# Performance work log

Measured on AMD Instinct MI355X. Metric: run time of the kernel, lower is better.

Reference implementation:

```python
import jax, jax.numpy as jnp
import numpy as np

B, N, DIM = 32, 3136, 64
H, DH, AGENTS = 8, 8, 49
INNER = H * DH  # 64
SCALE = DH ** -0.5


def setup_inputs() -> dict:
    key = jax.random.key(0)
    ks = jax.random.split(key, 7)
    s = 0.05
    return {
        "x1": jax.random.normal(ks[0], (B, N, DIM), jnp.float32),
        "x2": jax.random.normal(ks[1], (B, N, INNER), jnp.float32),
        "Wq": jax.random.normal(ks[2], (INNER, DIM), jnp.float32) * s,   # to_q (out,in)
        "Wk": jax.random.normal(ks[3], (DIM, INNER), jnp.float32) * s,   # to_k
        "Wv": jax.random.normal(ks[4], (DIM, INNER), jnp.float32) * s,   # to_v
        "Wo": jax.random.normal(ks[5], (2 * DIM, 2 * DIM), jnp.float32) * s,  # to_out linear
        "bo": jax.random.normal(ks[6], (2 * DIM,), jnp.float32) * s,
    }


def _split_heads(t):
    # (b, n, h*d) -> (b, h, n, d)
    b, n, hd = t.shape
    return t.reshape(b, n, H, hd // H).transpose(0, 2, 1, 3)


def reference(x1, x2, Wq, Wk, Wv, Wo, bo):
    b, n, _ = x1.shape
    q = x1 @ Wq.T                      # (b, n, 64)
    k = x2 @ Wk.T                      # (b, n, dim=64)
    v = x2 @ Wv.T
    # AdaptiveAvgPool2d((49, dim)): n % 49 == 0 and channel 64->64 is identity,
    # so pooling is an exact block mean over the sequence axis.
    agent = q.reshape(b, AGENTS, n // AGENTS, q.shape[-1]).mean(axis=2)  # (b, 49, 64)

    agent_h = _split_heads(agent)      # (b, h, 49, d)
    q1 = _split_heads(q)               # (b, h, n, d)
    k_h = _split_heads(k)
    v_h = _split_heads(v)

    # stage 0: agent tokens attend over keys/values (dropout is identity at eval)
    dots0 = jnp.einsum('bhid,bhjd->bhij', agent_h, k_h) * SCALE   # (b,h,49,n)
    attn0 = jax.nn.softmax(dots0, axis=-1)
    out0 = jnp.einsum('bhij,bhjd->bhid', attn0, v_h)              # (b,h,49,d)

    # stage 1: queries attend over agent tokens
    dots1 = jnp.einsum('bhid,bhjd->bhij', q1, agent_h) * SCALE    # (b,h,n,49)
    attn1 = jax.nn.softmax(dots1, axis=-1)
    out1 = jnp.einsum('bhij,bhjd->bhid', attn1, out0)             # (b,h,n,d)

    out1 = out1.transpose(0, 2, 1, 3).reshape(b, n, -1)           # (b,n,64)
    out1 = jnp.concatenate([out1, x1], axis=-1)                   # (b,n,128)
    return out1 @ Wo.T + bo
```

## Files before the change

### kernel.cpp

```cpp
#include <hip/hip_runtime.h>
#include <hip/hip_bf16.h>

#define NB 32
#define NSEQ 3136
#define NDIM 64
#define NH 8
#define NAG 49

static constexpr float kScale = 0.35355339059327378f;
static constexpr float kLog2e = 1.4426950408889634f;

typedef unsigned short us;
typedef __attribute__((ext_vector_type(8))) __bf16 bf16x8;
typedef __attribute__((ext_vector_type(4))) __bf16 bf16x4;
typedef __attribute__((ext_vector_type(2))) _Float16 f16x2;
typedef __attribute__((ext_vector_type(4))) _Float16 f16x4;
typedef __attribute__((ext_vector_type(8))) _Float16 f16x8;
typedef __attribute__((ext_vector_type(4))) float f32x4;

__device__ __forceinline__ float fexp2(float x) {
#if __has_builtin(__builtin_amdgcn_exp2f)
  return __builtin_amdgcn_exp2f(x);
#else
  return exp2f(x);
#endif
}

__device__ __forceinline__ float frcp(float x) {
#if __has_builtin(__builtin_amdgcn_rcpf)
  return __builtin_amdgcn_rcpf(x);
#else
  return 1.f / x;
#endif
}

__device__ __forceinline__ unsigned pk2(float a, float b) {
#if __has_builtin(__builtin_amdgcn_cvt_pkrtz)
  return __builtin_bit_cast(unsigned, __builtin_amdgcn_cvt_pkrtz(a, b));
#else
  f16x2 v = {(_Float16)a, (_Float16)b};
  return __builtin_bit_cast(unsigned, v);
#endif
}

__device__ __forceinline__ bf16x8 ldw8(const float* W, int row, int c0, int ld) {
  const float4* p = (const float4*)(W + (size_t)row * ld + c0);
  float4 v0 = p[0], v1 = p[1];
  bf16x8 r;
  r[0]=(__bf16)v0.x; r[1]=(__bf16)v0.y; r[2]=(__bf16)v0.z; r[3]=(__bf16)v0.w;
  r[4]=(__bf16)v1.x; r[5]=(__bf16)v1.y; r[6]=(__bf16)v1.z; r[7]=(__bf16)v1.w;
  return r;
}

__global__ __launch_bounds__(256) void agent_x1_kernel(
    const float* __restrict__ x1, const float* __restrict__ Wq,
    us* __restrict__ x1bf, us* __restrict__ agf16) {
  __shared__ float red[4][64];
  __shared__ float marr[64];
  const int a = blockIdx.x, b = blockIdx.y, t = threadIdx.x;
  const int i64 = t & 63, cb = t >> 6;

  {
    const float4* s1 = (const float4*)(x1 + ((size_t)(b * NSEQ) + a * 64 + i64) * NDIM + cb * 16);
    float4 v0 = s1[0], v1 = s1[1], v2 = s1[2], v3 = s1[3];
    bf16x8 p0, p1;
    p0[0]=(__bf16)v0.x; p0[1]=(__bf16)v0.y; p0[2]=(__bf16)v0.z; p0[3]=(__bf16)v0.w;
    p0[4]=(__bf16)v1.x; p0[5]=(__bf16)v1.y; p0[6]=(__bf16)v1.z; p0[7]=(__bf16)v1.w;
    p1[0]=(__bf16)v2.x; p1[1]=(__bf16)v2.y; p1[2]=(__bf16)v2.z; p1[3]=(__bf16)v2.w;
    p1[4]=(__bf16)v3.x; p1[5]=(__bf16)v3.y; p1[6]=(__bf16)v3.z; p1[7]=(__bf16)v3.w;
    __bf16* dst = (__bf16*)x1bf;
    *(bf16x8*)(dst + ((((size_t)b * NAG + a) * 8 + cb * 2) * 64 + i64) * 8) = p0;
    *(bf16x8*)(dst + ((((size_t)b * NAG + a) * 8 + cb * 2 + 1) * 64 + i64) * 8) = p1;
  }
  {
    const float* xc = x1 + ((size_t)(b * NSEQ) + a * 64 + cb * 16) * NDIM + i64;
    float cs = 0.f;
#pragma unroll
    for (int i = 0; i < 16; ++i) cs += xc[i * NDIM];
    red[cb][i64] = cs;
  }
  __syncthreads();
  if (t < 64) marr[t] = red[0][t] + red[1][t] + red[2][t] + red[3][t];
  __syncthreads();
  if (t < 64) {
    const float4* wqr = (const float4*)(Wq + (size_t)t * NDIM);
    const float4* mm = (const float4*)marr;
    float s0 = 0.f;
#pragma unroll
    for (int i = 0; i < 16; ++i) {
      float4 wv4 = wqr[i], m4 = mm[i];
      s0 += wv4.x * m4.x + wv4.y * m4.y + wv4.z * m4.z + wv4.w * m4.w;
    }
    const float val = s0 * (kScale * kLog2e / 64.f);
    ((_Float16*)agf16)[(((size_t)b * NH + (t >> 3)) * NAG + a) * 8 + (t & 7)] =
        (_Float16)val;
  }
}

__global__ __launch_bounds__(256) void kv_stage0_kernel(
    const float* __restrict__ x2, const float* __restrict__ Wk,
    const float* __restrict__ Wv, const us* __restrict__ agf16,
    float* __restrict__ pvp) {
  __shared__ __align__(16) __bf16 xb[64][72];
  __shared__ __align__(16) _Float16 klds[4][64][24];
  __shared__ __align__(16) _Float16 vlds[4][18][72];
  __shared__ __align__(16) _Float16 plds[4][64][40];
  const int a = blockIdx.x, b = blockIdx.y, t = threadIdx.x;
  const int i64 = t & 63, cb = t >> 6;
  const int w = cb, lr = (t >> 4) & 3, lc = t & 15;

  bf16x8 ak0 = ldw8(Wk, w * 16 + lc, lr * 8, NDIM);
  bf16x8 ak1 = ldw8(Wk, w * 16 + lc, 32 + lr * 8, NDIM);
  bf16x8 av0 = ldw8(Wv, w * 16 + lc, lr * 8, NDIM);
  bf16x8 av1 = ldw8(Wv, w * 16 + lc, 32 + lr * 8, NDIM);

  {
    const float4* s2 = (const float4*)(x2 + ((size_t)(b * NSEQ) + a * 64 + i64) * NDIM + cb * 16);
    float4 v0 = s2[0], v1 = s2[1], v2 = s2[2], v3 = s2[3];
    bf16x8 p0, p1;
    p0[0]=(__bf16)v0.x; p0[1]=(__bf16)v0.y; p0[2]=(__bf16)v0.z; p0[3]=(__bf16)v0.w;
    p0[4]=(__bf16)v1.x; p0[5]=(__bf16)v1.y; p0[6]=(__bf16)v1.z; p0[7]=(__bf16)v1.w;
    p1[0]=(__bf16)v2.x; p1[1]=(__bf16)v2.y; p1[2]=(__bf16)v2.z; p1[3]=(__bf16)v2.w;
    p1[4]=(__bf16)v3.x; p1[5]=(__bf16)v3.y; p1[6]=(__bf16)v3.z; p1[7]=(__bf16)v3.w;
    *(bf16x8*)&xb[i64][cb * 16] = p0; *(bf16x8*)&xb[i64][cb * 16 + 8] = p1;
  }
  __syncthreads();

  f32x4 acck[4], accv[4];
#pragma unroll
  for (int i = 0; i < 4; ++i) {
    acck[i] = (f32x4){0.f, 0.f, 0.f, 0.f};
    accv[i] = (f32x4){0.f, 0.f, 0.f, 0.f};
  }
#pragma unroll
  for (int nt = 0; nt < 4; ++nt) {
    bf16x8 x0 = *(const bf16x8*)&xb[nt * 16 + lc][lr * 8];
    bf16x8 x1f = *(const bf16x8*)&xb[nt * 16 + lc][32 + lr * 8];
    acck[nt] = __builtin_amdgcn_mfma_f32_16x16x32_bf16(ak0, x0, acck[nt], 0, 0, 0);
    acck[nt] = __builtin_amdgcn_mfma_f32_16x16x32_bf16(ak1, x1f, acck[nt], 0, 0, 0);
    accv[nt] = __builtin_amdgcn_mfma_f32_16x16x32_bf16(av0, x0, accv[nt], 0, 0, 0);
    accv[nt] = __builtin_amdgcn_mfma_f32_16x16x32_bf16(av1, x1f, accv[nt], 0, 0, 0);
  }
#pragma unroll
  for (int nt = 0; nt < 4; ++nt) {
    f16x4 pk4;
    pk4[0]=(_Float16)acck[nt][0]; pk4[1]=(_Float16)acck[nt][1];
    pk4[2]=(_Float16)acck[nt][2]; pk4[3]=(_Float16)acck[nt][3];
    *(f16x4*)&klds[w][nt * 16 + lc][lr * 4] = pk4;
#pragma unroll
    for (int j = 0; j < 4; ++j)
      vlds[w][lr * 4 + j][nt * 16 + lc] = (_Float16)accv[nt][j];
  }
  vlds[w][16][i64] = (_Float16)1.0f;

  const size_t bh0 = (size_t)b * NH + 2 * w;
  f16x8 ba[2][4];
#pragma unroll
  for (int hh = 0; hh < 2; ++hh)
#pragma unroll
    for (int at = 0; at < 4; ++at) {
      f16x8 v = (f16x8)(_Float16)0.0f;
      if (lr == 0) {
        int row = at * 16 + lc; if (row > 48) row = 48;
        v = *(const f16x8*)(agf16 + (bh0 + hh) * (NAG * 8) + row * 8);
      }
      ba[hh][at] = v;
    }

#pragma unroll
  for (int hh = 0; hh < 2; ++hh) {
    f32x4 accPV[4];
#pragma unroll
    for (int i = 0; i < 4; ++i) accPV[i] = (f32x4){0.f, 0.f, 0.f, 0.f};
#pragma unroll
    for (int half = 0; half < 2; ++half) {
#pragma unroll
      for (int tb = 0; tb < 2; ++tb) {
        const int tokbase = half * 32 + tb * 16;
        f16x8 kf = *(const f16x8*)&klds[w][tokbase + lc][hh * 8];
#pragma unroll
        for (int at = 0; at < 4; ++at) {
          f32x4 sc = __builtin_amdgcn_mfma_f32_16x16x32_f16(
              kf, ba[hh][at], (f32x4){0.f, 0.f, 0.f, 0.f}, 0, 0, 0);
          unsigned u0 = pk2(fexp2(sc[0]), fexp2(sc[1]));
          unsigned u1 = pk2(fexp2(sc[2]), fexp2(sc[3]));
          unsigned long long q = ((unsigned long long)u1 << 32) | u0;
          *(unsigned long long*)&plds[w][at * 16 + lc][tb * 16 + lr * 4] = q;
        }
      }
      const int frow = (lc < 8) ? hh * 8 + lc : 16;
      f16x8 vf = *(const f16x8*)&vlds[w][frow][half * 32 + lr * 8];
#pragma unroll
      for (int at = 0; at < 4; ++at) {
        f16x8 pf = *(const f16x8*)&plds[w][at * 16 + lc][lr * 8];
        accPV[at] = __builtin_amdgcn_mfma_f32_16x16x32_f16(pf, vf, accPV[at], 0, 0, 0);
      }
    }
    if (lc < 9) {
      float* dst = pvp + ((size_t)a * (NB * NH) + bh0 + hh) * 441;
#pragma unroll
      for (int at = 0; at < 4; ++at)
#pragma unroll
        for (int j = 0; j < 4; ++j) {
          const int ag = at * 16 + lr * 4 + j;
          if (ag < NAG) dst[ag * 9 + lc] = accPV[at][j];
        }
    }
  }
}

__global__ __launch_bounds__(256) void aofin_kernel(
    const float* __restrict__ pvp, us* __restrict__ pvtF) {
  __shared__ float acc[441];
  const int h = blockIdx.x, b = blockIdx.y, t = threadIdx.x;
  const size_t bh = (size_t)b * NH + h;
  for (int s = t; s < 441; s += 256) {
    float v = 0.f;
#pragma unroll 7
    for (int aa = 0; aa < NAG; ++aa)
      v += pvp[((size_t)aa * (NB * NH) + bh) * 441 + s];
    acc[s] = v;
  }
  __syncthreads();
  if (t < 64) {
    us* col = pvtF + bh * 1024 + t;
    float inv = (t < NAG) ? frcp(acc[t * 9 + 8]) : 0.f;
#pragma unroll
    for (int f = 0; f < 8; ++f) {
      float val = (t < NAG) ? acc[t * 9 + f] * inv : 0.f;
      _Float16 hv = (_Float16)val;
      col[f * 64] = __builtin_bit_cast(us, hv);
    }
    col[8 * 64] = (t < NAG) ? (us)0x3C00 : (us)0;
#pragma unroll
    for (int f = 9; f < 16; ++f) col[f * 64] = 0;
  }
}

__global__ __launch_bounds__(512, 6) void stage1_out_kernel(
    const us* __restrict__ x1bf, const float* __restrict__ x1,
    const float* __restrict__ Wq, const us* __restrict__ agf16,
    const us* __restrict__ pvtF, const float* __restrict__ Wo,
    const float* __restrict__ bo, float* __restrict__ out) {
  __shared__ __align__(16) __bf16 xa[64][72];
  __shared__ __align__(16) us qcat[64][72];
  __shared__ __align__(16) _Float16 pW[8][16][104];
  const int tile = blockIdx.x, b = blockIdx.y;
  const int t = threadIdx.x, tokl = t & 63, h = t >> 6;
  const int w = h, lane = t & 63, lr = (lane >> 4) & 3, lc = lane & 15;
  const int mtile = w & 3, thalf = w >> 2;
  const size_t bh = (size_t)b * NH + w;

  bf16x8 wqf0 = ldw8(Wq, mtile * 16 + lc, lr * 8, NDIM);
  bf16x8 wqf1 = ldw8(Wq, mtile * 16 + lc, 32 + lr * 8, NDIM);

  f16x8 ba[4];
#pragma unroll
  for (int at = 0; at < 4; ++at) {
    f16x8 v = (f16x8)(_Float16)0.0f;
    if (lr == 0) {
      int row = at * 16 + lc; if (row > 48) row = 48;
      v = *(const f16x8*)(agf16 + bh * (NAG * 8) + row * 8);
    }
    ba[at] = v;
  }
  const us* pvb = pvtF + bh * 1024;
  f16x8 pvB0 = *(const f16x8*)(pvb + lc * 64 + lr * 8);
  f16x8 pvB1 = *(const f16x8*)(pvb + lc * 64 + 32 + lr * 8);

  {
    bf16x8 p = *(const bf16x8*)((const __bf16*)x1bf +
        ((((size_t)b * NAG + tile) * 8 + h) * 64 + tokl) * 8);
    *(bf16x8*)&xa[tokl][h * 8] = p;
  }
  __syncthreads();

  {
    f32x4 aq[2];
    aq[0] = (f32x4){0.f,0.f,0.f,0.f}; aq[1] = (f32x4){0.f,0.f,0.f,0.f};
#pragma unroll
    for (int nt = 0; nt < 2; ++nt) {
      bf16x8 bx0 = *(const bf16x8*)&xa[thalf * 32 + nt * 16 + lc][lr * 8];
      bf16x8 bx1 = *(const bf16x8*)&xa[thalf * 32 + nt * 16 + lc][32 + lr * 8];
      aq[nt] = __builtin_amdgcn_mfma_f32_16x16x32_bf16(wqf0, bx0, aq[nt], 0, 0, 0);
      aq[nt] = __builtin_amdgcn_mfma_f32_16x16x32_bf16(wqf1, bx1, aq[nt], 0, 0, 0);
    }
#pragma unroll
    for (int nt = 0; nt < 2; ++nt) {
      f16x4 pk;
      pk[0]=(_Float16)aq[nt][0]; pk[1]=(_Float16)aq[nt][1];
      pk[2]=(_Float16)aq[nt][2]; pk[3]=(_Float16)aq[nt][3];
      *(f16x4*)&qcat[thalf * 32 + nt * 16 + lc][mtile * 16 + lr * 4] = pk;
    }
  }
  __syncthreads();

  {
    _Float16* psw = &pW[w][0][0];
#pragma unroll 1
    for (int g = 0; g < 4; ++g) {
      f16x8 qf = *(const f16x8*)&qcat[g * 16 + lc][w * 8];
#pragma unroll
      for (int at = 0; at < 4; ++at) {
        f32x4 sc = __builtin_amdgcn_mfma_f32_16x16x32_f16(
            ba[at], qf, (f32x4){0.f, 0.f, 0.f, 0.f}, 0, 0, 0);
        unsigned u0 = pk2(fexp2(sc[0]), fexp2(sc[1]));
        unsigned u1 = pk2(fexp2(sc[2]), fexp2(sc[3]));
        unsigned long long qq = ((unsigned long long)u1 << 32) | u0;
        *(unsigned long long*)&psw[(size_t)lc * 104 + at * 16 + lr * 4] = qq;
      }
      f16x8 pA0 = *(const f16x8*)&psw[(size_t)lc * 104 + lr * 8];
      f16x8 pA1 = *(const f16x8*)&psw[(size_t)lc * 104 + 32 + lr * 8];
      f32x4 pv = __builtin_amdgcn_mfma_f32_16x16x32_f16(
          pvB0, pA0, (f32x4){0.f, 0.f, 0.f, 0.f}, 0, 0, 0);
      pv = __builtin_amdgcn_mfma_f32_16x16x32_f16(pvB1, pA1, pv, 0, 0, 0);
      float den = __shfl(pv[0], 32 + lc);
      float inv = frcp(den);
      if (lr < 2) {
        bf16x4 pc;
        pc[0] = (__bf16)(pv[0] * inv); pc[1] = (__bf16)(pv[1] * inv);
        pc[2] = (__bf16)(pv[2] * inv); pc[3] = (__bf16)(pv[3] * inv);
        *(bf16x4*)((__bf16*)&qcat[g * 16 + lc][0] + w * 8 + lr * 4) = pc;
      }
    }
  }
  bf16x8 wof[4];
#pragma unroll
  for (int ks = 0; ks < 4; ++ks)
    wof[ks] = ldw8(Wo, w * 16 + lc, ks * 32 + lr * 8, 128);
  f32x4 bv = *(const f32x4*)(bo + w * 16 + lr * 4);
  __syncthreads();

  {
    f32x4 acc[4];
#pragma unroll
    for (int i = 0; i < 4; ++i) acc[i] = (f32x4){0.f,0.f,0.f,0.f};
#pragma unroll
    for (int ks = 0; ks < 4; ++ks) {
#pragma unroll
      for (int nt = 0; nt < 4; ++nt) {
        bf16x8 bx = (ks < 2) ? *(const bf16x8*)&qcat[nt * 16 + lc][ks * 32 + lr * 8]
                             : *(const bf16x8*)&xa[nt * 16 + lc][(ks - 2) * 32 + lr * 8];
        acc[nt] = __builtin_amdgcn_mfma_f32_16x16x32_bf16(wof[ks], bx, acc[nt], 0, 0, 0);
      }
    }
#pragma unroll
    for (int nt = 0; nt < 4; ++nt) {
      f32x4 v = acc[nt] + bv;
      float* dst = out + ((size_t)b * NSEQ + tile * 64 + nt * 16 + lc) * 128 + w * 16 + lr * 4;
      *(f32x4*)dst = v;
    }
  }
  (void)x1;
}

extern "C" void kernel_launch(void* const* d_in, const int* in_sizes, int n_in,
                              void* d_out, int out_size, void* d_ws, size_t ws_size,
                              hipStream_t stream) {
  (void)in_sizes; (void)n_in; (void)out_size; (void)ws_size;
  const float* x1 = (const float*)d_in[0];
  const float* x2 = (const float*)d_in[1];
  const float* Wq = (const float*)d_in[2];
  const float* Wk = (const float*)d_in[3];
  const float* Wv = (const float*)d_in[4];
  const float* Wo = (const float*)d_in[5];
  const float* bo = (const float*)d_in[6];
  float* out = (float*)d_out;

  us* x1bf = (us*)d_ws;
  us* agf16 = x1bf + (size_t)NB * NSEQ * 64;
  float* pvp = (float*)(agf16 + (size_t)NB * NH * NAG * 8);
  us* pvtF = (us*)(pvp + (size_t)NAG * NB * NH * 441);

  agent_x1_kernel<<<dim3(NAG, NB), 256, 0, stream>>>(x1, Wq, x1bf, agf16);
  kv_stage0_kernel<<<dim3(NAG, NB), 256, 0, stream>>>(x2, Wk, Wv, agf16, pvp);
  aofin_kernel<<<dim3(NH, NB), 256, 0, stream>>>(pvp, pvtF);
  stage1_out_kernel<<<dim3(NAG, NB), 512, 0, stream>>>(x1bf, x1, Wq, agf16,
                                                       pvtF, Wo, bo, out);
}
```

Baseline: 78.70 us.

## Replace partial-sum buffer and reduce kernel with atomic accumulation

Stage-0 partial PV results are now accumulated directly into a single per-(batch,head) buffer with float atomicAdd, instead of being written per agent-tile and summed by a separate reduction kernel. That buffer is zeroed inside the first kernel. The normalization and fp16 packing that the removed kernel did are folded into the stage-1 kernel's fragment load. This drops one launch and a large round-trip through the partials buffer. In exchange it adds atomic contention across 49 tiles per address, makes the sums order-nondeterministic, and makes every stage-1 block recompute reciprocals.

Result: slower. 114.2 us (+45.1%).

```diff
diff --git a/kernel.cpp b/kernel.cpp
--- a/kernel.cpp
+++ b/kernel.cpp
@@ -54,11 +54,16 @@
 
 __global__ __launch_bounds__(256) void agent_x1_kernel(
     const float* __restrict__ x1, const float* __restrict__ Wq,
-    us* __restrict__ x1bf, us* __restrict__ agf16) {
+    us* __restrict__ x1bf, us* __restrict__ agf16, float* __restrict__ pvs) {
   __shared__ float red[4][64];
   __shared__ float marr[64];
   const int a = blockIdx.x, b = blockIdx.y, t = threadIdx.x;
   const int i64 = t & 63, cb = t >> 6;
+
+  if (a == 0) {
+    float* pz = pvs + (size_t)b * (NH * 441);
+    for (int i = t; i < NH * 441; i += 256) pz[i] = 0.f;
+  }
 
   {
     const float4* s1 = (const float4*)(x1 + ((size_t)(b * NSEQ) + a * 64 + i64) * NDIM + cb * 16);
@@ -100,7 +105,7 @@
 __global__ __launch_bounds__(256) void kv_stage0_kernel(
     const float* __restrict__ x2, const float* __restrict__ Wk,
     const float* __restrict__ Wv, const us* __restrict__ agf16,
-    float* __restrict__ pvp) {
+    float* __restrict__ pvs) {
   __shared__ __align__(16) __bf16 xb[64][72];
   __shared__ __align__(16) _Float16 klds[4][64][24];
   __shared__ __align__(16) _Float16 vlds[4][18][72];
@@ -197,51 +202,23 @@
       }
     }
     if (lc < 9) {
-      float* dst = pvp + ((size_t)a * (NB * NH) + bh0 + hh) * 441;
+      float* dst = pvs + (bh0 + hh) * 441;
 #pragma unroll
       for (int at = 0; at < 4; ++at)
 #pragma unroll
         for (int j = 0; j < 4; ++j) {
           const int ag = at * 16 + lr * 4 + j;
-          if (ag < NAG) dst[ag * 9 + lc] = accPV[at][j];
+          if (ag < NAG) atomicAdd(&dst[ag * 9 + lc], accPV[at][j]);
         }
     }
   }
 }
 
-__global__ __launch_bounds__(256) void aofin_kernel(
-    const float* __restrict__ pvp, us* __restrict__ pvtF) {
-  __shared__ float acc[441];
-  const int h = blockIdx.x, b = blockIdx.y, t = threadIdx.x;
-  const size_t bh = (size_t)b * NH + h;
-  for (int s = t; s < 441; s += 256) {
-    float v = 0.f;
-#pragma unroll 7
-    for (int aa = 0; aa < NAG; ++aa)
-      v += pvp[((size_t)aa * (NB * NH) + bh) * 441 + s];
-    acc[s] = v;
-  }
-  __syncthreads();
-  if (t < 64) {
-    us* col = pvtF + bh * 1024 + t;
-    float inv = (t < NAG) ? frcp(acc[t * 9 + 8]) : 0.f;
-#pragma unroll
-    for (int f = 0; f < 8; ++f) {
-      float val = (t < NAG) ? acc[t * 9 + f] * inv : 0.f;
-      _Float16 hv = (_Float16)val;
-      col[f * 64] = __builtin_bit_cast(us, hv);
-    }
-    col[8 * 64] = (t < NAG) ? (us)0x3C00 : (us)0;
-#pragma unroll
-    for (int f = 9; f < 16; ++f) col[f * 64] = 0;
-  }
-}
-
 __global__ __launch_bounds__(512, 6) void stage1_out_kernel(
-    const us* __restrict__ x1bf, const float* __restrict__ x1,
-    const float* __restrict__ Wq, const us* __restrict__ agf16,
-    const us* __restrict__ pvtF, const float* __restrict__ Wo,
-    const float* __restrict__ bo, float* __restrict__ out) {
+    const us* __restrict__ x1bf, const float* __restrict__ Wq,
+    const us* __restrict__ agf16, const float* __restrict__ pvs,
+    const float* __restrict__ Wo, const float* __restrict__ bo,
+    float* __restrict__ out) {
   __shared__ __align__(16) __bf16 xa[64][72];
   __shared__ __align__(16) us qcat[64][72];
   __shared__ __align__(16) _Float16 pW[8][16][104];
@@ -264,9 +241,26 @@
     }
     ba[at] = v;
   }
-  const us* pvb = pvtF + bh * 1024;
-  f16x8 pvB0 = *(const f16x8*)(pvb + lc * 64 + lr * 8);
-  f16x8 pvB1 = *(const f16x8*)(pvb + lc * 64 + 32 + lr * 8);
+  f16x8 pvB0, pvB1;
+  {
+    const float* pvsb = pvs + bh * 441;
+#pragma unroll
+    for (int i = 0; i < 8; ++i) {
+      const int ag0 = lr * 8 + i;
+      const int ag1 = 32 + lr * 8 + i;
+      float v0, v1;
+      if (lc < 8) {
+        v0 = pvsb[ag0 * 9 + lc] * frcp(pvsb[ag0 * 9 + 8]);
+        v1 = (ag1 < NAG) ? pvsb[ag1 * 9 + lc] * frcp(pvsb[ag1 * 9 + 8]) : 0.f;
+      } else if (lc == 8) {
+        v0 = 1.f; v1 = (ag1 < NAG) ? 1.f : 0.f;
+      } else {
+        v0 = 0.f; v1 = 0.f;
+      }
+      pvB0[i] = (_Float16)v0;
+      pvB1[i] = (_Float16)v1;
+    }
+  }
 
   {
     bf16x8 p = *(const bf16x8*)((const __bf16*)x1bf +
@@ -351,7 +345,6 @@
       *(f32x4*)dst = v;
     }
   }
-  (void)x1;
 }
 
 extern "C" void kernel_launch(void* const* d_in, const int* in_sizes, int n_in,
@@ -369,12 +362,10 @@
 
   us* x1bf = (us*)d_ws;
   us* agf16 = x1bf + (size_t)NB * NSEQ * 64;
-  float* pvp = (float*)(agf16 + (size_t)NB * NH * NAG * 8);
-  us* pvtF = (us*)(pvp + (size_t)NAG * NB * NH * 441);
-
-  agent_x1_kernel<<<dim3(NAG, NB), 256, 0, stream>>>(x1, Wq, x1bf, agf16);
-  kv_stage0_kernel<<<dim3(NAG, NB), 256, 0, stream>>>(x2, Wk, Wv, agf16, pvp);
-  aofin_kernel<<<dim3(NH, NB), 256, 0, stream>>>(pvp, pvtF);
-  stage1_out_kernel<<<dim3(NAG, NB), 512, 0, stream>>>(x1bf, x1, Wq, agf16,
-                                                       pvtF, Wo, bo, out);
-}
+  float* pvs = (float*)(agf16 + (size_t)NB * NH * NAG * 8);
+
+  agent_x1_kernel<<<dim3(NAG, NB), 256, 0, stream>>>(x1, Wq, x1bf, agf16, pvs);
+  kv_stage0_kernel<<<dim3(NAG, NB), 256, 0, stream>>>(x2, Wk, Wv, agf16, pvs);
+  stage1_out_kernel<<<dim3(NAG, NB), 512, 0, stream>>>(x1bf, Wq, agf16, pvs,
+                                                       Wo, bo, out);
+}
```
